# Kernel tuning notes

Hardware: AMD Instinct MI355X
Metric: run time of the kernel (lower is better)

## Reference

```python
import jax, jax.numpy as jnp
import numpy as np

N_NODES = 100000
N_EDGES = 500000
IN_DIM, HID, N_CLS = 128, 512, 40


def gcn_conv(x, W, b, src, dst, num_nodes):
    # PyG GCNConv: h = x W; add self-loops; norm = d^-1/2[src] * d^-1/2[dst];
    # out[dst] += norm * h[src]; out += bias
    h = x @ W  # [N, out_dim]
    ones = jnp.ones(src.shape[0], dtype=x.dtype)
    deg = jax.ops.segment_sum(ones, dst, num_segments=num_nodes)  # in-degree incl self-loops
    dinv = jnp.where(deg > 0, jax.lax.rsqrt(deg), 0.0)
    norm = dinv[src] * dinv[dst]  # [E]
    msgs = h[src] * norm[:, None]  # [E, out_dim] gather + scale
    out = jax.ops.segment_sum(msgs, dst, num_segments=num_nodes)
    return out + b


def setup_inputs() -> dict:
    key = jax.random.key(0)
    k1, k2, k3, k4, k5, k6 = jax.random.split(key, 6)
    x = jax.random.normal(k1, (N_NODES, IN_DIM), dtype=jnp.float32)
    edge_index = jax.random.randint(k2, (2, N_EDGES), 0, N_NODES, dtype=jnp.int32)
    # Glorot-ish params
    W1 = jax.random.normal(k3, (IN_DIM, HID), dtype=jnp.float32) * (1.0 / np.sqrt(IN_DIM))
    b1 = jnp.zeros((HID,), dtype=jnp.float32)
    W2 = jax.random.normal(k4, (HID, N_CLS), dtype=jnp.float32) * (1.0 / np.sqrt(HID))
    b2 = jnp.zeros((N_CLS,), dtype=jnp.float32)
    return {"x": x, "edge_index": edge_index, "W1": W1, "b1": b1, "W2": W2, "b2": b2}


def reference(x, edge_index, W1, b1, W2, b2):
    n = x.shape[0]
    # add self-loops once, shared by both conv layers
    loop = jnp.arange(n, dtype=edge_index.dtype)
    src = jnp.concatenate([edge_index[0], loop])
    dst = jnp.concatenate([edge_index[1], loop])
    h = gcn_conv(x, W1, b1, src, dst, n)
    h = jax.nn.relu(h)
    # dropout is identity in eval mode (reference computed in eval)
    h = gcn_conv(h, W2, b2, src, dst, n)
    return jax.nn.log_softmax(h, axis=1)
```

## Files before the change

kernel.cpp:

```cpp
#include <hip/hip_runtime.h>
#include <cstdint>
#include <cstddef>

#define N_NODES 100000
#define N_EDGES 500000
#define IN_DIM  128
#define HID     512
#define N_CLS   40
#define SEG     32
#define N_ZBLK  ((N_NODES + 255) / 256)
#define N_CNTB  ((N_EDGES + 255) / 256)
#define N_XBFB  12500
#define N_G1B   6250
#define N_PREPB 352

typedef short bf16x8 __attribute__((ext_vector_type(8)));
typedef float f32x4 __attribute__((ext_vector_type(4)));

__device__ inline unsigned short f2bf(float f) {
  unsigned u = __float_as_uint(f);
  u = u + 0x7fffu + ((u >> 16) & 1u);
  return (unsigned short)(u >> 16);
}
__device__ inline float blo(unsigned u) { return __uint_as_float(u << 16); }
__device__ inline float bhi(unsigned u) { return __uint_as_float(u & 0xffff0000u); }

__global__ __launch_bounds__(256) void k_zero(int* __restrict__ cnt) {
  int i = blockIdx.x * 256 + threadIdx.x;
  if (i < N_NODES) cnt[i] = 0;
}

__global__ __launch_bounds__(256) void k_count(const int* __restrict__ dst, int* __restrict__ cnt,
                                               int* __restrict__ rank) {
  int e = blockIdx.x * 256 + threadIdx.x;
  if (e < N_EDGES) rank[e] = atomicAdd(&cnt[dst[e]], 1);
}

__global__ __launch_bounds__(256) void k_fill_xbf(const int* __restrict__ src, const int* __restrict__ dst,
                                                  const int* __restrict__ rank, const int* __restrict__ cnt,
                                                  int2* __restrict__ epair,
                                                  const float* __restrict__ x, uint2* __restrict__ xb2) {
  int b = blockIdx.x;
  if (b < N_CNTB) {
    int e = b * 256 + threadIdx.x;
    if (e >= N_EDGES) return;
    int s = src[e], d = dst[e];
    int pos = d * SEG + rank[e];
    float nrm = rsqrtf((float)(cnt[s] + 1)) * rsqrtf((float)(cnt[d] + 1));
    epair[pos] = make_int2(s, __float_as_int(nrm));
  } else {
    int t = (b - N_CNTB) * 256 + threadIdx.x;
    float4 v = ((const float4*)x)[t];
    uint2 o;
    o.x = (unsigned)f2bf(v.x) | ((unsigned)f2bf(v.y) << 16);
    o.y = (unsigned)f2bf(v.z) | ((unsigned)f2bf(v.w) << 16);
    xb2[t] = o;
  }
}

#define ACC8(A, n, R) \
  A##0 += (n) * blo((R).x); A##1 += (n) * bhi((R).x); \
  A##2 += (n) * blo((R).y); A##3 += (n) * bhi((R).y); \
  A##4 += (n) * blo((R).z); A##5 += (n) * bhi((R).z); \
  A##6 += (n) * blo((R).w); A##7 += (n) * bhi((R).w);

__global__ __launch_bounds__(256) void k_gather1(const uint4* __restrict__ xb4, const int2* __restrict__ ep,
                                                 const int* __restrict__ cnt,
                                                 uint4* __restrict__ z1,
                                                 const float* __restrict__ W1, const float* __restrict__ W2,
                                                 unsigned short* __restrict__ W1F, unsigned short* __restrict__ W2F) {
  int b = blockIdx.x;
  if (b >= N_G1B) {
    int t = (b - N_G1B) * 256 + threadIdx.x;
    if (t < 65536) {
      int j = t & 7, lane = (t >> 3) & 63, rest = t >> 9;
      int kfrag = rest & 3, c = rest >> 2;
      int k = kfrag * 32 + ((lane >> 4) & 3) * 8 + j;
      int i = lane & 15;
      int h = (c >> 1) * 32 + (i >> 2) * 8 + (c & 1) * 4 + (i & 3);
      W1F[t] = f2bf(W1[k * HID + h]);
    } else {
      int u = t - 65536;
      int j = u & 7, lane = (u >> 3) & 63, rest = u >> 9;
      int ct = rest % 3, gk = rest / 3;
      int k = gk * 32 + ((lane >> 4) & 3) * 8 + j;
      int col = ct * 16 + (lane & 15);
      W2F[u] = (col < N_CLS) ? f2bf(W2[k * N_CLS + col]) : (unsigned short)0;
    }
    return;
  }
  int lane = threadIdx.x & 63, qq = lane >> 4, l = lane & 15;
  int d = b * 16 + (threadIdx.x >> 6) * 4 + qq;
  int cd = cnt[d];
  int start = d * SEG, end = start + cd;
  float dd = rsqrtf((float)(cd + 1)), sl = dd * dd;
  uint4 su = xb4[(size_t)d * 16 + l];
  float a0 = sl * blo(su.x), a1 = sl * bhi(su.x), a2 = sl * blo(su.y), a3 = sl * bhi(su.y);
  float a4 = sl * blo(su.z), a5 = sl * bhi(su.z), a6 = sl * blo(su.w), a7 = sl * bhi(su.w);
  float p0 = 0.f, p1 = 0.f, p2 = 0.f, p3 = 0.f, p4 = 0.f, p5 = 0.f, p6 = 0.f, p7 = 0.f;
  float q0 = 0.f, q1 = 0.f, q2 = 0.f, q3 = 0.f, q4 = 0.f, q5 = 0.f, q6 = 0.f, q7 = 0.f;
  float r0 = 0.f, r1 = 0.f, r2 = 0.f, r3 = 0.f, r4 = 0.f, r5 = 0.f, r6 = 0.f, r7 = 0.f;

  int last = end - 1;
  for (int i0 = start; i0 < end; i0 += 8) {
    int rem = end - i0;
    int j1 = (rem > 1) ? i0 + 1 : last;
    int j2 = (rem > 2) ? i0 + 2 : last;
    int j3 = (rem > 3) ? i0 + 3 : last;
    int j4 = (rem > 4) ? i0 + 4 : last;
    int j5 = (rem > 5) ? i0 + 5 : last;
    int j6 = (rem > 6) ? i0 + 6 : last;
    int j7 = (rem > 7) ? i0 + 7 : last;
    int2 e0 = ep[i0], e1 = ep[j1], e2 = ep[j2], e3 = ep[j3];
    int2 e4 = ep[j4], e5 = ep[j5], e6 = ep[j6], e7 = ep[j7];
    uint4 x0 = xb4[(size_t)e0.x * 16 + l];
    uint4 x1 = xb4[(size_t)e1.x * 16 + l];
    uint4 x2 = xb4[(size_t)e2.x * 16 + l];
    uint4 x3 = xb4[(size_t)e3.x * 16 + l];
    uint4 x4 = xb4[(size_t)e4.x * 16 + l];
    uint4 x5 = xb4[(size_t)e5.x * 16 + l];
    uint4 x6 = xb4[(size_t)e6.x * 16 + l];
    uint4 x7 = xb4[(size_t)e7.x * 16 + l];
    float n0 = __int_as_float(e0.y);
    float n1 = (rem > 1) ? __int_as_float(e1.y) : 0.f;
    float n2 = (rem > 2) ? __int_as_float(e2.y) : 0.f;
    float n3 = (rem > 3) ? __int_as_float(e3.y) : 0.f;
    float n4 = (rem > 4) ? __int_as_float(e4.y) : 0.f;
    float n5 = (rem > 5) ? __int_as_float(e5.y) : 0.f;
    float n6 = (rem > 6) ? __int_as_float(e6.y) : 0.f;
    float n7 = (rem > 7) ? __int_as_float(e7.y) : 0.f;
    ACC8(a, n0, x0)
    ACC8(p, n1, x1)
    ACC8(q, n2, x2)
    ACC8(r, n3, x3)
    ACC8(a, n4, x4)
    ACC8(p, n5, x5)
    ACC8(q, n6, x6)
    ACC8(r, n7, x7)
  }
  a0 += p0 + q0 + r0;  a1 += p1 + q1 + r1;
  a2 += p2 + q2 + r2;  a3 += p3 + q3 + r3;
  a4 += p4 + q4 + r4;  a5 += p5 + q5 + r5;
  a6 += p6 + q6 + r6;  a7 += p7 + q7 + r7;
  uint4 o;
  o.x = (unsigned)f2bf(a0) | ((unsigned)f2bf(a1) << 16);
  o.y = (unsigned)f2bf(a2) | ((unsigned)f2bf(a3) << 16);
  o.z = (unsigned)f2bf(a4) | ((unsigned)f2bf(a5) << 16);
  o.w = (unsigned)f2bf(a6) | ((unsigned)f2bf(a7) << 16);
  z1[(size_t)d * 16 + l] = o;
}

__global__ __launch_bounds__(64) void k_fused_mfma(const unsigned short* __restrict__ z1b,
                                                   const unsigned short* __restrict__ W1F,
                                                   const float* __restrict__ b1,
                                                   const unsigned short* __restrict__ W2F,
                                                   unsigned short* __restrict__ Pb) {
  const int lane = threadIdx.x;
  const int c16  = lane & 15, quad = lane >> 4;
  const int mbase = blockIdx.x * 32;

  bf16x8 afrag[2][4];
  #pragma unroll
  for (int t = 0; t < 2; ++t) {
    int mrow = mbase + t * 16 + c16;
    const bf16x8* arow = (const bf16x8*)(z1b + (size_t)mrow * IN_DIM + quad * 8);
    afrag[t][0] = arow[0];
    afrag[t][1] = arow[4];
    afrag[t][2] = arow[8];
    afrag[t][3] = arow[12];
  }

  f32x4 pacc[2][3];
  #pragma unroll
  for (int t = 0; t < 2; ++t)
    #pragma unroll
    for (int ct = 0; ct < 3; ++ct) pacc[t][ct] = (f32x4){0.f, 0.f, 0.f, 0.f};

  const bf16x8* w1f = (const bf16x8*)W1F;
  const bf16x8* w2f = (const bf16x8*)W2F;
  const float4* b1v = (const float4*)b1;

  for (int g = 0; g < 16; ++g) {
    bf16x8 wa[8];
    #pragma unroll
    for (int f = 0; f < 8; ++f) wa[f] = w1f[(g * 8 + f) * 64 + lane];
    bf16x8 wb[3];
    #pragma unroll
    for (int ct = 0; ct < 3; ++ct) wb[ct] = w2f[(g * 3 + ct) * 64 + lane];
    float4 bb0 = b1v[g * 8 + quad * 2 + 0];
    float4 bb1 = b1v[g * 8 + quad * 2 + 1];

    #pragma unroll
    for (int t = 0; t < 2; ++t) {
      f32x4 h0 = (f32x4){0.f, 0.f, 0.f, 0.f};
      f32x4 h1 = (f32x4){0.f, 0.f, 0.f, 0.f};
      #pragma unroll
      for (int k = 0; k < 4; ++k)
        h0 = __builtin_amdgcn_mfma_f32_16x16x32_bf16(wa[k], afrag[t][k], h0, 0, 0, 0);
      #pragma unroll
      for (int k = 0; k < 4; ++k)
        h1 = __builtin_amdgcn_mfma_f32_16x16x32_bf16(wa[4 + k], afrag[t][k], h1, 0, 0, 0);
      float e0 = fmaxf(h0[0] + bb0.x, 0.f), e1 = fmaxf(h0[1] + bb0.y, 0.f);
      float e2 = fmaxf(h0[2] + bb0.z, 0.f), e3 = fmaxf(h0[3] + bb0.w, 0.f);
      float f0 = fmaxf(h1[0] + bb1.x, 0.f), f1 = fmaxf(h1[1] + bb1.y, 0.f);
      float f2 = fmaxf(h1[2] + bb1.z, 0.f), f3 = fmaxf(h1[3] + bb1.w, 0.f);
      unsigned q0, q1, q2, q3;
      asm("v_cvt_pk_bf16_f32 %0, %1, %2" : "=v"(q0) : "v"(e0), "v"(e1));
      asm("v_cvt_pk_bf16_f32 %0, %1, %2" : "=v"(q1) : "v"(e2), "v"(e3));
      asm("v_cvt_pk_bf16_f32 %0, %1, %2" : "=v"(q2) : "v"(f0), "v"(f1));
      asm("v_cvt_pk_bf16_f32 %0, %1, %2" : "=v"(q3) : "v"(f2), "v"(f3));
      union { unsigned u[4]; bf16x8 v; } pa;
      pa.u[0] = q0; pa.u[1] = q1; pa.u[2] = q2; pa.u[3] = q3;
      #pragma unroll
      for (int ct = 0; ct < 3; ++ct)
        pacc[t][ct] = __builtin_amdgcn_mfma_f32_16x16x32_bf16(pa.v, wb[ct], pacc[t][ct], 0, 0, 0);
    }
  }

  #pragma unroll
  for (int t = 0; t < 2; ++t) {
    int mrow0 = mbase + t * 16 + quad * 4;
    #pragma unroll
    for (int ct = 0; ct < 3; ++ct) {
      int col = ct * 16 + c16;
      if (col < N_CLS) {
        #pragma unroll
        for (int r = 0; r < 4; ++r) {
          int m = mrow0 + r;
          Pb[(size_t)m * N_CLS + col] = f2bf(pacc[t][ct][r]);
        }
      }
    }
  }
}

#define ACC4(A, n, U) \
  A##0a += (n) * blo((U).x); A##1a += (n) * bhi((U).x); \
  A##2a += (n) * blo((U).y); A##3a += (n) * bhi((U).y);

__global__ __launch_bounds__(256) void k_gather2_lsm(const uint2* __restrict__ Pu2,
                                                     const int2* __restrict__ ep,
                                                     const int* __restrict__ cnt,
                                                     const float* __restrict__ b2,
                                                     float* __restrict__ out) {
  int lane = threadIdx.x & 63, q = lane >> 4, l = lane & 15;
  int d = blockIdx.x * 16 + (threadIdx.x >> 6) * 4 + q;
  bool act = l < 10;
  int lc = act ? l : 0;
  int cd = cnt[d];
  int start = d * SEG, end = start + cd;
  float dd = rsqrtf((float)(cd + 1)), sl = dd * dd;

  uint2 su = Pu2[(size_t)d * 10 + lc];
  float a0a = sl * blo(su.x), a1a = sl * bhi(su.x), a2a = sl * blo(su.y), a3a = sl * bhi(su.y);
  float p0a = 0.f, p1a = 0.f, p2a = 0.f, p3a = 0.f;
  float q0a = 0.f, q1a = 0.f, q2a = 0.f, q3a = 0.f;
  float r0a = 0.f, r1a = 0.f, r2a = 0.f, r3a = 0.f;

  int last = end - 1;
  for (int i0 = start; i0 < end; i0 += 8) {
    int rem = end - i0;
    int j1 = (rem > 1) ? i0 + 1 : last;
    int j2 = (rem > 2) ? i0 + 2 : last;
    int j3 = (rem > 3) ? i0 + 3 : last;
    int j4 = (rem > 4) ? i0 + 4 : last;
    int j5 = (rem > 5) ? i0 + 5 : last;
    int j6 = (rem > 6) ? i0 + 6 : last;
    int j7 = (rem > 7) ? i0 + 7 : last;
    int2 e0 = ep[i0], e1 = ep[j1], e2 = ep[j2], e3 = ep[j3];
    int2 e4 = ep[j4], e5 = ep[j5], e6 = ep[j6], e7 = ep[j7];
    uint2 u0 = Pu2[(size_t)e0.x * 10 + lc];
    uint2 u1 = Pu2[(size_t)e1.x * 10 + lc];
    uint2 u2 = Pu2[(size_t)e2.x * 10 + lc];
    uint2 u3 = Pu2[(size_t)e3.x * 10 + lc];
    uint2 u4 = Pu2[(size_t)e4.x * 10 + lc];
    uint2 u5 = Pu2[(size_t)e5.x * 10 + lc];
    uint2 u6 = Pu2[(size_t)e6.x * 10 + lc];
    uint2 u7 = Pu2[(size_t)e7.x * 10 + lc];
    float n0 = __int_as_float(e0.y);
    float n1 = (rem > 1) ? __int_as_float(e1.y) : 0.f;
    float n2 = (rem > 2) ? __int_as_float(e2.y) : 0.f;
    float n3 = (rem > 3) ? __int_as_float(e3.y) : 0.f;
    float n4 = (rem > 4) ? __int_as_float(e4.y) : 0.f;
    float n5 = (rem > 5) ? __int_as_float(e5.y) : 0.f;
    float n6 = (rem > 6) ? __int_as_float(e6.y) : 0.f;
    float n7 = (rem > 7) ? __int_as_float(e7.y) : 0.f;
    ACC4(a, n0, u0)
    ACC4(p, n1, u1)
    ACC4(q, n2, u2)
    ACC4(r, n3, u3)
    ACC4(a, n4, u4)
    ACC4(p, n5, u5)
    ACC4(q, n6, u6)
    ACC4(r, n7, u7)
  }

  float v0, v1, v2, v3;
  if (act) {
    float4 bb = ((const float4*)b2)[l];
    v0 = a0a + p0a + q0a + r0a + bb.x;
    v1 = a1a + p1a + q1a + r1a + bb.y;
    v2 = a2a + p2a + q2a + r2a + bb.z;
    v3 = a3a + p3a + q3a + r3a + bb.w;
  } else {
    v0 = v1 = v2 = v3 = -1e30f;
  }
  float m = fmaxf(fmaxf(v0, v1), fmaxf(v2, v3));
  #pragma unroll
  for (int off = 8; off > 0; off >>= 1) m = fmaxf(m, __shfl_xor(m, off, 64));
  float e = act ? (expf(v0 - m) + expf(v1 - m) + expf(v2 - m) + expf(v3 - m)) : 0.f;
  float s = e;
  #pragma unroll
  for (int off = 8; off > 0; off >>= 1) s += __shfl_xor(s, off, 64);
  float lse = m + logf(s);
  if (act) {
    float4 o = make_float4(v0 - lse, v1 - lse, v2 - lse, v3 - lse);
    ((float4*)(out + (size_t)d * N_CLS))[l] = o;
  }
}

extern "C" void kernel_launch(void* const* d_in, const int* in_sizes, int n_in,
                              void* d_out, int out_size, void* d_ws, size_t ws_size,
                              hipStream_t stream) {
  const float* x  = (const float*)d_in[0];
  const int*   ei = (const int*)d_in[1];
  const int*  src = ei;
  const int*  dst = ei + N_EDGES;
  const float* W1 = (const float*)d_in[2];
  const float* b1 = (const float*)d_in[3];
  const float* W2 = (const float*)d_in[4];
  const float* b2 = (const float*)d_in[5];
  float* out = (float*)d_out;

  int*   cnt     = (int*)d_ws;
  int*   rank    = cnt + 131072;
  int2*  epair   = (int2*)(rank + 524288);
  uint2* xb2     = (uint2*)(epair + (size_t)N_NODES * SEG);
  unsigned short* Pb = (unsigned short*)xb2;
  unsigned short* z1b = (unsigned short*)(xb2 + 3200000);
  unsigned short* W1F = z1b + (size_t)N_NODES * IN_DIM;
  unsigned short* W2F = W1F + HID * IN_DIM;

  k_zero    <<<N_ZBLK, 256, 0, stream>>>(cnt);
  k_count   <<<N_CNTB, 256, 0, stream>>>(dst, cnt, rank);
  k_fill_xbf<<<N_CNTB + N_XBFB, 256, 0, stream>>>(src, dst, rank, cnt, epair, x, xb2);
  k_gather1 <<<N_G1B + N_PREPB, 256, 0, stream>>>((const uint4*)xb2, epair, cnt,
                                                  (uint4*)z1b, W1, W2, W1F, W2F);
  k_fused_mfma<<<N_NODES / 32, 64, 0, stream>>>(z1b, W1F, b1, W2F, Pb);
  k_gather2_lsm<<<N_NODES / 16, 256, 0, stream>>>((const uint2*)Pb, epair, cnt, b2, out);
}
```

Baseline: 207.0 us.

## Share W1/W2 fragments via double-buffered LDS across four waves in fused MFMA

The fused MFMA kernel now runs 256-thread blocks of four waves, each covering 32 rows, so one block handles 128 nodes. Per-group W1/W2 weight fragments are staged once per block into double-buffered shared memory, with the next group's fragments prefetched into registers. Previously every single-wave block read the whole weight set from global memory or L2 itself. The change adds two block barriers per group and bounds checks for the partial last block.

```diff
diff --git a/kernel.cpp b/kernel.cpp
--- a/kernel.cpp
+++ b/kernel.cpp
@@ -13,6 +13,7 @@
 #define N_XBFB  12500
 #define N_G1B   6250
 #define N_PREPB 352
+#define N_MFMB  ((N_NODES + 127) / 128)
 
 typedef short bf16x8 __attribute__((ext_vector_type(8)));
 typedef float f32x4 __attribute__((ext_vector_type(4)));
@@ -150,20 +151,23 @@
   z1[(size_t)d * 16 + l] = o;
 }
 
-__global__ __launch_bounds__(64) void k_fused_mfma(const unsigned short* __restrict__ z1b,
-                                                   const unsigned short* __restrict__ W1F,
-                                                   const float* __restrict__ b1,
-                                                   const unsigned short* __restrict__ W2F,
-                                                   unsigned short* __restrict__ Pb) {
-  const int lane = threadIdx.x;
+__global__ __launch_bounds__(256) void k_fused_mfma(const unsigned short* __restrict__ z1b,
+                                                    const unsigned short* __restrict__ W1F,
+                                                    const float* __restrict__ b1,
+                                                    const unsigned short* __restrict__ W2F,
+                                                    unsigned short* __restrict__ Pb) {
+  __shared__ uint4 Bs[2][704];
+  const int tid  = threadIdx.x;
+  const int w    = tid >> 6, lane = tid & 63;
   const int c16  = lane & 15, quad = lane >> 4;
-  const int mbase = blockIdx.x * 32;
+  const int mbase = blockIdx.x * 128 + w * 32;
 
   bf16x8 afrag[2][4];
   #pragma unroll
   for (int t = 0; t < 2; ++t) {
     int mrow = mbase + t * 16 + c16;
-    const bf16x8* arow = (const bf16x8*)(z1b + (size_t)mrow * IN_DIM + quad * 8);
+    int meff = (mrow < N_NODES) ? mrow : 0;
+    const bf16x8* arow = (const bf16x8*)(z1b + (size_t)meff * IN_DIM + quad * 8);
     afrag[t][0] = arow[0];
     afrag[t][1] = arow[4];
     afrag[t][2] = arow[8];
@@ -176,17 +180,31 @@
     #pragma unroll
     for (int ct = 0; ct < 3; ++ct) pacc[t][ct] = (f32x4){0.f, 0.f, 0.f, 0.f};
 
-  const bf16x8* w1f = (const bf16x8*)W1F;
-  const bf16x8* w2f = (const bf16x8*)W2F;
+  const uint4* w1g = (const uint4*)W1F;
+  const uint4* w2g = (const uint4*)W2F;
   const float4* b1v = (const float4*)b1;
+  const int t2 = (tid < 192) ? tid : 191;
+
+  Bs[0][tid]       = w1g[tid];
+  Bs[0][tid + 256] = w1g[256 + tid];
+  if (tid < 192) Bs[0][512 + tid] = w2g[t2];
+  __syncthreads();
 
   for (int g = 0; g < 16; ++g) {
+    const int cur = g & 1;
+    const int gn = (g < 15) ? g + 1 : 15;
+    uint4 s0 = w1g[gn * 512 + tid];
+    uint4 s1 = w1g[gn * 512 + 256 + tid];
+    uint4 s2 = w2g[gn * 192 + t2];
+
+    const bf16x8* waf = (const bf16x8*)(&Bs[cur][0]);
+    const bf16x8* wbf = (const bf16x8*)(&Bs[cur][512]);
     bf16x8 wa[8];
     #pragma unroll
-    for (int f = 0; f < 8; ++f) wa[f] = w1f[(g * 8 + f) * 64 + lane];
+    for (int f = 0; f < 8; ++f) wa[f] = waf[f * 64 + lane];
     bf16x8 wb[3];
     #pragma unroll
-    for (int ct = 0; ct < 3; ++ct) wb[ct] = w2f[(g * 3 + ct) * 64 + lane];
+    for (int ct = 0; ct < 3; ++ct) wb[ct] = wbf[ct * 64 + lane];
     float4 bb0 = b1v[g * 8 + quad * 2 + 0];
     float4 bb1 = b1v[g * 8 + quad * 2 + 1];
 
@@ -215,6 +233,15 @@
       for (int ct = 0; ct < 3; ++ct)
         pacc[t][ct] = __builtin_amdgcn_mfma_f32_16x16x32_bf16(pa.v, wb[ct], pacc[t][ct], 0, 0, 0);
     }
+
+    if (g < 15) {
+      __syncthreads();
+      const int nb = cur ^ 1;
+      Bs[nb][tid]       = s0;
+      Bs[nb][tid + 256] = s1;
+      if (tid < 192) Bs[nb][512 + tid] = s2;
+      __syncthreads();
+    }
   }
 
   #pragma unroll
@@ -227,7 +254,7 @@
         #pragma unroll
         for (int r = 0; r < 4; ++r) {
           int m = mrow0 + r;
-          Pb[(size_t)m * N_CLS + col] = f2bf(pacc[t][ct][r]);
+          if (m < N_NODES) Pb[(size_t)m * N_CLS + col] = f2bf(pacc[t][ct][r]);
         }
       }
     }
@@ -346,6 +373,6 @@
   k_fill_xbf<<<N_CNTB + N_XBFB, 256, 0, stream>>>(src, dst, rank, cnt, epair, x, xb2);
   k_gather1 <<<N_G1B + N_PREPB, 256, 0, stream>>>((const uint4*)xb2, epair, cnt,
                                                   (uint4*)z1b, W1, W2, W1F, W2F);
-  k_fused_mfma<<<N_NODES / 32, 64, 0, stream>>>(z1b, W1F, b1, W2F, Pb);
+  k_fused_mfma<<<N_MFMB, 256, 0, stream>>>(z1b, W1F, b1, W2F, Pb);
   k_gather2_lsm<<<N_NODES / 16, 256, 0, stream>>>((const uint2*)Pb, epair, cnt, b2, out);
 }
```

Result: slower. 212.8 us (+2.8%).
